# Kernel tuning notes

Hardware: AMD Instinct MI355X
Metric: run time of the kernel (lower is better)

Reference implementation:

```python
import jax, jax.numpy as jnp
import numpy as np

B, S, D = 4, 2048, 1024
H = 4 * D          # expert hidden dim
E_SPEC = 4         # num specific experts
E_SHR = 2          # num shared experts
TOP_K = 2


def setup_inputs() -> dict:
    key = jax.random.key(0)
    ks = jax.random.split(key, 16)
    s = 0.02
    return {
        "x": jax.random.normal(ks[0], (B, S, D), jnp.float32),
        # specific experts (stacked over expert axis)
        "spec_w1": jax.random.normal(ks[1], (E_SPEC, D, H), jnp.float32) * s,
        "spec_b1": jnp.zeros((E_SPEC, H), jnp.float32),
        "spec_w2": jax.random.normal(ks[2], (E_SPEC, H, D), jnp.float32) * s,
        "spec_b2": jnp.zeros((E_SPEC, D), jnp.float32),
        "spec_rw": jax.random.normal(ks[3], (D, E_SPEC), jnp.float32) * s,
        "spec_rb": jnp.zeros((E_SPEC,), jnp.float32),
        # shared experts
        "shr_w1": jax.random.normal(ks[4], (E_SHR, D, H), jnp.float32) * s,
        "shr_b1": jnp.zeros((E_SHR, H), jnp.float32),
        "shr_w2": jax.random.normal(ks[5], (E_SHR, H, D), jnp.float32) * s,
        "shr_b2": jnp.zeros((E_SHR, D), jnp.float32),
        "shr_rw": jax.random.normal(ks[6], (D, E_SHR), jnp.float32) * s,
        "shr_rb": jnp.zeros((E_SHR,), jnp.float32),
    }


def _expert_mlp(xf, w1, b1, w2, b2):
    # xf: [T, D]; w1: [E, D, H]; w2: [E, H, D] -> [E, T, D]
    h = jax.nn.gelu(jnp.einsum("td,edh->eth", xf, w1) + b1[:, None, :],
                    approximate=False)
    return jnp.einsum("eth,ehd->etd", h, w2) + b2[:, None, :]


def reference(x, spec_w1, spec_b1, spec_w2, spec_b2, spec_rw, spec_rb,
              shr_w1, shr_b1, shr_w2, shr_b2, shr_rw, shr_rb):
    b, s, d = x.shape
    xf = x.reshape(-1, d)                      # [T, D]
    T = xf.shape[0]

    # --- specific (top-k) routing ---
    spec_probs = jax.nn.softmax(xf @ spec_rw + spec_rb, axis=-1)   # [T, E]
    topk_probs, topk_idx = jax.lax.top_k(spec_probs, TOP_K)        # [T, K]

    # aux load-balancing loss
    counts = jnp.zeros((E_SPEC,), jnp.float32).at[topk_idx.reshape(-1)].add(1.0)
    fraction = counts / (T * TOP_K)
    aux_loss = E_SPEC * jnp.sum(fraction * spec_probs.mean(axis=0))

    # gate[t, e] = sum_k topk_probs[t,k] * 1[topk_idx[t,k]==e]
    gate = jnp.sum(jax.nn.one_hot(topk_idx, E_SPEC, dtype=xf.dtype)
                   * topk_probs[..., None], axis=1)                # [T, E]

    spec_out_e = _expert_mlp(xf, spec_w1, spec_b1, spec_w2, spec_b2)  # [E, T, D]
    specific_out = jnp.einsum("te,etd->td", gate, spec_out_e)

    # --- shared (dense) experts ---
    shr_probs = jax.nn.softmax(xf @ shr_rw + shr_rb, axis=-1)      # [T, E_shr]
    shr_out_e = _expert_mlp(xf, shr_w1, shr_b1, shr_w2, shr_b2)    # [E_shr, T, D]
    shared_out = jnp.einsum("te,etd->td", shr_probs, shr_out_e)

    final = (specific_out + shared_out).reshape(b, s, d)
    return final, aux_loss
```

## Files before the change

### kernel.cpp

```cpp
#include <hip/hip_runtime.h>
#include <hip/hip_bf16.h>

#define T_TOK 8192
#define DDIM 1024
#define HDIM 4096

typedef __bf16 bf16;
typedef bf16 bf16x8 __attribute__((ext_vector_type(8)));
typedef float f32x4 __attribute__((ext_vector_type(4)));

#define ASM_VMCNT(n) asm volatile("s_waitcnt vmcnt(" #n ")" ::: "memory")
#define MFMA16(a, b, c) __builtin_amdgcn_mfma_f32_16x16x32_bf16((a), (b), (c), 0, 0, 0)

__device__ __forceinline__ void gl_lds16(const void* g, void* l) {
  __builtin_amdgcn_global_load_lds(
      (const __attribute__((address_space(1))) unsigned int*)g,
      (__attribute__((address_space(3))) unsigned int*)l, 16, 0, 0);
}

__device__ __forceinline__ float gelu_f(float v) {
  const float x = v * 0.7071067811865475f;
  const float ax = fabsf(x);
  const float t = 1.0f / fmaf(0.3275911f, ax, 1.0f);
  float p = fmaf(1.061405429f, t, -1.453152027f);
  p = fmaf(p, t, 1.421413741f);
  p = fmaf(p, t, -0.284496736f);
  p = fmaf(p, t, 0.254829592f);
  p = p * t;
  const float e = __expf(-ax * ax);
  const float er = fmaf(-p, e, 1.0f);
  const float erfx = (x >= 0.0f) ? er : -er;
  return 0.5f * v * (1.0f + erfx);
}

__global__ __launch_bounds__(256) void conv_router(
    const float* __restrict__ x, bf16* __restrict__ xb,
    const float* __restrict__ srw, const float* __restrict__ srb,
    const float* __restrict__ hrw, const float* __restrict__ hrb,
    float* __restrict__ gate, float4* __restrict__ probs4,
    int* __restrict__ top2) {
  const int lane = threadIdx.x & 63;
  const int w = threadIdx.x >> 6;
  const int t = blockIdx.x * 4 + w;

  const float* xr = x + (size_t)t * DDIM;
  bf16* xbr = xb + (size_t)t * DDIM;
  float p0 = 0, p1 = 0, p2 = 0, p3 = 0, p4 = 0, p5 = 0;
#pragma unroll
  for (int c = 0; c < 4; ++c) {
    const int d = c * 256 + lane * 4;
    const float4 xv = *(const float4*)(xr + d);
    bf16 ov[4] = {(bf16)xv.x, (bf16)xv.y, (bf16)xv.z, (bf16)xv.w};
    *(float2*)(xbr + d) = *(float2*)ov;
    const float xa[4] = {xv.x, xv.y, xv.z, xv.w};
#pragma unroll
    for (int j = 0; j < 4; ++j) {
      const float xd = xa[j];
      const float4 r4 = *(const float4*)(srw + (size_t)(d + j) * 4);
      p0 += xd * r4.x; p1 += xd * r4.y; p2 += xd * r4.z; p3 += xd * r4.w;
      const float2 r2 = *(const float2*)(hrw + (size_t)(d + j) * 2);
      p4 += xd * r2.x; p5 += xd * r2.y;
    }
  }
#pragma unroll
  for (int off = 32; off >= 1; off >>= 1) {
    p0 += __shfl_xor(p0, off);
    p1 += __shfl_xor(p1, off);
    p2 += __shfl_xor(p2, off);
    p3 += __shfl_xor(p3, off);
    p4 += __shfl_xor(p4, off);
    p5 += __shfl_xor(p5, off);
  }
  if (lane == 0) {
    const float l0 = p0 + srb[0], l1 = p1 + srb[1];
    const float l2 = p2 + srb[2], l3 = p3 + srb[3];
    const float m = fmaxf(fmaxf(l0, l1), fmaxf(l2, l3));
    const float e0 = expf(l0 - m), e1 = expf(l1 - m);
    const float e2 = expf(l2 - m), e3 = expf(l3 - m);
    const float s = e0 + e1 + e2 + e3;
    float pr[4] = {e0 / s, e1 / s, e2 / s, e3 / s};
    int i1 = 0; float v1 = pr[0];
#pragma unroll
    for (int e = 1; e < 4; ++e) if (pr[e] > v1) { v1 = pr[e]; i1 = e; }
    int i2 = -1; float v2 = -1.0f;
#pragma unroll
    for (int e = 0; e < 4; ++e)
      if (e != i1 && pr[e] > v2) { v2 = pr[e]; i2 = e; }
    float g[4] = {0, 0, 0, 0};
    g[i1] = v1; g[i2] = v2;
    float* gr = gate + (size_t)t * 8;
    gr[0] = g[0]; gr[1] = g[1]; gr[2] = g[2]; gr[3] = g[3];
    const float h0 = p4 + hrb[0], h1 = p5 + hrb[1];
    const float mh = fmaxf(h0, h1);
    const float q0 = expf(h0 - mh), q1 = expf(h1 - mh);
    const float qs = q0 + q1;
    gr[4] = q0 / qs; gr[5] = q1 / qs; gr[6] = 0; gr[7] = 0;
    probs4[t] = make_float4(pr[0], pr[1], pr[2], pr[3]);
    top2[t] = i1 | (i2 << 8);
  }
}

__global__ __launch_bounds__(256) void transpose_convert(
    const float* __restrict__ src, bf16* __restrict__ dst, int R, int C) {
  __shared__ float tile[32][33];
  const size_t mat = (size_t)blockIdx.z * R * C;
  const int c0 = blockIdx.x * 32, r0 = blockIdx.y * 32;
  const int tx = threadIdx.x & 31, ty = threadIdx.x >> 5;
#pragma unroll
  for (int i = 0; i < 4; ++i)
    tile[ty + 8 * i][tx] =
        src[mat + (size_t)(r0 + ty + 8 * i) * C + c0 + tx];
  __syncthreads();
#pragma unroll
  for (int i = 0; i < 4; ++i)
    dst[mat + (size_t)(c0 + ty + 8 * i) * R + r0 + tx] =
        (bf16)tile[tx][ty + 8 * i];
}

__global__ __launch_bounds__(1024) void scan_build(
    const int* __restrict__ top2, const float4* __restrict__ probs4,
    int* __restrict__ cnt, int* __restrict__ lists, float* __restrict__ auxg) {
  __shared__ unsigned long long sc[1024];
  __shared__ float4 rp[512];
  const int tid = threadIdx.x;

  int ee[8];
  unsigned long long c = 0;
  float4 ps = make_float4(0.f, 0.f, 0.f, 0.f);
#pragma unroll
  for (int j = 0; j < 8; ++j) {
    const int t = tid * 8 + j;
    const int p = top2[t];
    ee[j] = p;
    const int a = p & 15, b = (p >> 8) & 15;
    c += (1ULL << (16 * a)) + (1ULL << (16 * b));
    const float4 pv = probs4[t];
    ps.x += pv.x; ps.y += pv.y; ps.z += pv.z; ps.w += pv.w;
  }
  sc[tid] = c;
  __syncthreads();
  for (int off = 1; off < 1024; off <<= 1) {
    const unsigned long long mine = sc[tid];
    const unsigned long long prev = (tid >= off) ? sc[tid - off] : 0ULL;
    __syncthreads();
    sc[tid] = mine + prev;
    __syncthreads();
  }
  const unsigned long long incl = sc[tid];
  const unsigned long long tot = sc[1023];
  const unsigned long long excl = incl - c;
  int q0 = (int)(excl & 0xffff), q1 = (int)((excl >> 16) & 0xffff);
  int q2 = (int)((excl >> 32) & 0xffff), q3 = (int)((excl >> 48) & 0xffff);
#pragma unroll
  for (int j = 0; j < 8; ++j) {
    const int t = tid * 8 + j;
    const int a = ee[j] & 15, b = (ee[j] >> 8) & 15;
    const int pa = (a == 0) ? q0 : (a == 1) ? q1 : (a == 2) ? q2 : q3;
    lists[a * 8192 + pa] = t;
    q0 += (a == 0); q1 += (a == 1); q2 += (a == 2); q3 += (a == 3);
    const int pb = (b == 0) ? q0 : (b == 1) ? q1 : (b == 2) ? q2 : q3;
    lists[b * 8192 + pb] = t;
    q0 += (b == 0); q1 += (b == 1); q2 += (b == 2); q3 += (b == 3);
  }
  if (tid == 1023) {
    const int c0 = (int)(tot & 0xffff), c1 = (int)((tot >> 16) & 0xffff);
    const int c2 = (int)((tot >> 32) & 0xffff), c3 = (int)((tot >> 48) & 0xffff);
    cnt[0] = c0; cnt[1] = c1; cnt[2] = c2; cnt[3] = c3;
    auxg[0] = (float)c0; auxg[1] = (float)c1;
    auxg[2] = (float)c2; auxg[3] = (float)c3;
  }
  if (tid >= 512) rp[tid - 512] = ps;
  __syncthreads();
  if (tid < 512) {
    const float4 o = rp[tid];
    ps.x += o.x; ps.y += o.y; ps.z += o.z; ps.w += o.w;
  }
  for (int w = 256; w >= 1; w >>= 1) {
    __syncthreads();
    if (tid >= w && tid < 2 * w) rp[tid - w] = ps;
    __syncthreads();
    if (tid < w) {
      const float4 o = rp[tid];
      ps.x += o.x; ps.y += o.y; ps.z += o.z; ps.w += o.w;
    }
  }
  if (tid == 0) {
    auxg[4] = ps.x; auxg[5] = ps.y; auxg[6] = ps.z; auxg[7] = ps.w;
  }
}

__global__ void aux_finalize(const float* __restrict__ auxg,
                             float* __restrict__ outp) {
  float a = 0.0f;
#pragma unroll
  for (int e = 0; e < 4; ++e)
    a += (auxg[e] / (float)(T_TOK * 2)) * (auxg[4 + e] / (float)T_TOK);
  outp[0] = 4.0f * a;
}

template <int MODE>
__global__ __launch_bounds__(256, 2) void gemmw(
    const bf16* __restrict__ A, const bf16* __restrict__ B, int N, int K,
    const float* __restrict__ bias, bf16* __restrict__ Hout, int NBn,
    int CH_M, int CH_N, const int* __restrict__ cnt,
    const int* __restrict__ lists, int eid) {
  __shared__ __align__(1024) bf16 As[3 * 256 * 32];
  __shared__ __align__(1024) bf16 Bs[3 * 128 * 32];

  const int tid = threadIdx.x;
  const int lane = tid & 63, wid = tid >> 6;
  const int wm = wid >> 1, wn = wid & 1;
  const int lr = lane & 15, lg = lane >> 4;

  int bm, bn;
  if constexpr (MODE == 4) {
    const int nbm = ((cnt[eid] + 255) & ~255) >> 8;
    const int CHm = (nbm + 3) >> 2;
    const int need = 8 * CHm * CH_N;
    if (blockIdx.x >= need) return;
    const int xc = blockIdx.x & 7;
    const int idx = blockIdx.x >> 3;
    bm = (xc >> 1) * CHm + idx / CH_N;
    bn = (xc & 1) * CH_N + idx % CH_N;
    if (bm >= nbm) return;
  } else {
    const int xcd = blockIdx.x & 7;
    const int idx = blockIdx.x >> 3;
    const int ncn = NBn / CH_N;
    bm = (xcd / ncn) * CH_M + idx / CH_N;
    bn = (xcd % ncn) * CH_N + idx % CH_N;
  }

  const int rl = tid >> 2;
  const int c = ((tid & 3) * 16) ^ (((rl >> 1) & 3) << 4);
  int ar0 = bm * 256 + rl, ar1 = ar0 + 64, ar2 = ar0 + 128, ar3 = ar0 + 192;
  if constexpr (MODE == 4) {
    const int* lp = lists + eid * 8192;
    int t;
    t = lp[ar0]; ar0 = t < 0 ? 0 : t;
    t = lp[ar1]; ar1 = t < 0 ? 0 : t;
    t = lp[ar2]; ar2 = t < 0 ? 0 : t;
    t = lp[ar3]; ar3 = t < 0 ? 0 : t;
  }
  const bf16* sA0 = A + (size_t)ar0 * K + (c >> 1);
  const bf16* sA1 = A + (size_t)ar1 * K + (c >> 1);
  const bf16* sA2 = A + (size_t)ar2 * K + (c >> 1);
  const bf16* sA3 = A + (size_t)ar3 * K + (c >> 1);
  const bf16* sB0 = B + (size_t)(bn * 128 + rl) * K + (c >> 1);
  const bf16* sB1 = B + (size_t)(bn * 128 + 64 + rl) * K + (c >> 1);

  char* const dA = (char*)As + wid * 1024;
  char* const dB = (char*)Bs + wid * 1024;

  const int rkey = ((lr >> 1) & 3) << 4;
  const char* Ard = (const char*)As + (wm * 128 + lr) * 64 + ((lg * 16) ^ rkey);
  const char* Brd = (const char*)Bs + (wn * 64 + lr) * 64 + ((lg * 16) ^ rkey);

  f32x4 acc[8][4] = {};
  const int NT = K >> 5;

#define GW_STAGE(KO, SLOT)                         \
  gl_lds16(sA0 + (KO), dA + (SLOT)*16384);         \
  gl_lds16(sA1 + (KO), dA + (SLOT)*16384 + 4096);  \
  gl_lds16(sA2 + (KO), dA + (SLOT)*16384 + 8192);  \
  gl_lds16(sA3 + (KO), dA + (SLOT)*16384 + 12288); \
  gl_lds16(sB0 + (KO), dB + (SLOT)*8192);          \
  gl_lds16(sB1 + (KO), dB + (SLOT)*8192 + 4096);
  GW_STAGE(0, 0)
  GW_STAGE(32, 1)
  GW_STAGE(64, 2)
  ASM_VMCNT(12);
  __builtin_amdgcn_s_barrier();

#define GW_ITER(KT, SLOT)                                                  \
  {                                                                        \
    bf16x8 af[8], bfr[4];                                                  \
    _Pragma("unroll") for (int mf = 0; mf < 8; ++mf)                       \
        af[mf] = *(const bf16x8*)(Ard + (SLOT)*16384 + mf * 1024);         \
    _Pragma("unroll") for (int nf = 0; nf < 4; ++nf)                       \
        bfr[nf] = *(const bf16x8*)(Brd + (SLOT)*8192 + nf * 1024);         \
    asm volatile("s_waitcnt lgkmcnt(0)" ::: "memory");                     \
    __builtin_amdgcn_s_setprio(1);                                         \
    _Pragma("unroll") for (int mf = 0; mf < 8; ++mf)                       \
        _Pragma("unroll") for (int nf = 0; nf < 4; ++nf)                   \
            acc[mf][nf] = MFMA16(af[mf], bfr[nf], acc[mf][nf]);            \
    __builtin_amdgcn_s_setprio(0);                                         \
    __builtin_amdgcn_s_barrier();                                          \
    if ((KT) + 3 < NT) {                                                   \
      const int ko_ = ((KT) + 3) << 5;                                     \
      GW_STAGE(ko_, SLOT)                                                  \
      ASM_VMCNT(12);                                                       \
    } else if ((KT) + 2 < NT) {                                            \
      ASM_VMCNT(6);                                                        \
    } else if ((KT) + 1 < NT) {                                            \
      ASM_VMCNT(0);                                                        \
    }                                                                      \
    __builtin_amdgcn_s_barrier();                                          \
  }

  for (int kt0 = 0; kt0 < NT; kt0 += 3) {
    GW_ITER(kt0, 0)
    if (kt0 + 1 < NT) GW_ITER(kt0 + 1, 1)
    if (kt0 + 2 < NT) GW_ITER(kt0 + 2, 2)
  }

  const int colb = bn * 128 + wn * 64;
  const int rowb = bm * 256 + wm * 128 + lg * 4;
  float bv[4];
#pragma unroll
  for (int nf = 0; nf < 4; ++nf) bv[nf] = bias[colb + nf * 16 + lr];
#pragma unroll
  for (int mf = 0; mf < 8; ++mf)
#pragma unroll
    for (int nf = 0; nf < 4; ++nf) {
      const int col = colb + nf * 16 + lr;
#pragma unroll
      for (int r = 0; r < 4; ++r) {
        const int row = rowb + mf * 16 + r;
        Hout[(size_t)row * N + col] = (bf16)gelu_f(acc[mf][nf][r] + bv[nf]);
      }
    }
}

template <int BN_, int MODE>
__global__ __launch_bounds__(512, 2) void gemm4p(
    const bf16* __restrict__ A, const bf16* __restrict__ B, int M, int N,
    int K, const float* __restrict__ bias, bf16* __restrict__ Hout,
    float* __restrict__ Fout, const float* __restrict__ gate, int gidx,
    int NBn, int CH_M, int CH_N, const int* __restrict__ cnt,
    const int* __restrict__ lists, int eid) {
  constexpr int NREP = BN_ / 64;
  constexpr int NHF = NREP / 2;
  constexpr int WNT = BN_ / 4;
  constexpr int ABYTES = 256 * 64 * 2;
  constexpr int BBYTES = BN_ * 64 * 2;
  constexpr bool DYN = (MODE == 3);

  __shared__ __align__(1024) bf16 Alds[2 * 256 * 64];
  __shared__ __align__(1024) bf16 Blds[2 * BN_ * 64];

  const int tid = threadIdx.x;
  const int lane = tid & 63, wid = tid >> 6;
  const int wm = wid >> 2, wn = wid & 3;
  const int lr = lane & 15, lg = lane >> 4;

  int bm, bn;
  if constexpr (DYN) {
    const int nbm = ((cnt[eid] + 255) & ~255) >> 8;
    const int CHm = (nbm + 3) >> 2;
    constexpr int CHn = (BN_ == 256) ? 8 : 4;
    const int need = 8 * CHm * CHn;
    if (blockIdx.x >= need) return;
    const int xc = blockIdx.x & 7;
    const int idx = blockIdx.x >> 3;
    bm = (xc >> 1) * CHm + idx / CHn;
    bn = (xc & 1) * CHn + idx % CHn;
    if (bm >= nbm) return;
  } else {
    const int xcd = blockIdx.x & 7;
    const int idx = blockIdx.x >> 3;
    const int ncn = NBn / CH_N;
    bm = (xcd / ncn) * CH_M + idx / CH_N;
    bn = (xcd % ncn) * CH_N + idx % CH_N;
  }

  const int NT = K >> 6;

  const int L = tid * 16;
  const int rl = L >> 7;
  const int colb = (L & 127) ^ ((rl & 7) << 4);

  const int ar0 = bm * 256 + rl;
  const bf16* sAc0 = A + (size_t)ar0 * K + (colb >> 1);
  const bf16* sAc1 = A + (size_t)(ar0 + 64) * K + (colb >> 1);
  const bf16* sAc2 = A + (size_t)(ar0 + 128) * K + (colb >> 1);
  const bf16* sAc3 = A + (size_t)(ar0 + 192) * K + (colb >> 1);
  const bf16* sB = B + (size_t)(bn * BN_ + rl) * K + (colb >> 1);

  char* const ldsA = (char*)Alds;
  char* const ldsB = (char*)Blds;
  const int wb = wid * 1024;
  char* const stA[2] = {ldsA + wb, ldsA + ABYTES + wb};
  char* const stB[2] = {ldsB + wb, ldsB + BBYTES + wb};

  const int ax0 = (lg * 16) ^ ((lr & 7) << 4);
  const int ax1 = ax0 ^ 64;
  const int aro = (wm * 128 + lr) * 128;
  const int bro = (wn * WNT + lr) * 128;
  const char* const Ak0[2] = {ldsA + aro + ax0, ldsA + ABYTES + aro + ax0};
  const char* const Ak1[2] = {ldsA + aro + ax1, ldsA + ABYTES + aro + ax1};
  const char* const Bk0[2] = {ldsB + bro + ax0, ldsB + BBYTES + bro + ax0};
  const char* const Bk1[2] = {ldsB + bro + ax1, ldsB + BBYTES + bro + ax1};

  f32x4 acc[8][NREP] = {};

  gl_lds16(sAc0, stA[0]);
  gl_lds16(sAc1, stA[0] + 8192);
  gl_lds16(sAc2, stA[0] + 16384);
  gl_lds16(sAc3, stA[0] + 24576);
  gl_lds16(sB, stB[0]);
  gl_lds16(sB + (size_t)64 * K, stB[0] + 8192);
  if constexpr (BN_ == 256) {
    gl_lds16(sB + (size_t)128 * K, stB[0] + 16384);
    gl_lds16(sB + (size_t)192 * K, stB[0] + 24576);
  }
  gl_lds16(sB + 64, stB[1]);
  gl_lds16(sB + (size_t)64 * K + 64, stB[1] + 8192);
  if constexpr (BN_ == 256) {
    gl_lds16(sB + (size_t)128 * K + 64, stB[1] + 16384);
    gl_lds16(sB + (size_t)192 * K + 64, stB[1] + 24576);
  }
  gl_lds16(sAc0 + 64, stA[1]);
  gl_lds16(sAc1 + 64, stA[1] + 8192);
  if constexpr (BN_ == 256) ASM_VMCNT(6); else ASM_VMCNT(4);
  __builtin_amdgcn_s_barrier();

  for (int kt0 = 0; kt0 < NT; kt0 += 2) {
#pragma unroll
    for (int par = 0; par < 2; ++par) {
      const int kt = kt0 + par;
      const int cur = par, oth = par ^ 1;
      const bool st1 = (kt + 1) < NT, st2 = (kt + 2) < NT;
      const size_t ko1 = (size_t)(kt + 1) << 6, ko2 = (size_t)(kt + 2) << 6;
      const char* Ac0 = Ak0[cur]; const char* Ac1 = Ak1[cur];
      const char* Bc0 = Bk0[cur]; const char* Bc1 = Bk1[cur];

      bf16x8 af[4][2], bfr[NREP][2];

#pragma unroll
      for (int mf = 0; mf < 4; ++mf) {
        af[mf][0] = *(const bf16x8*)(Ac0 + mf * 2048);
        af[mf][1] = *(const bf16x8*)(Ac1 + mf * 2048);
      }
#pragma unroll
      for (int nf = 0; nf < NHF; ++nf) {
        bfr[nf][0] = *(const bf16x8*)(Bc0 + nf * 2048);
        bfr[nf][1] = *(const bf16x8*)(Bc1 + nf * 2048);
      }
      if (st1) {
        gl_lds16(sAc2 + ko1, stA[oth] + 16384);
        gl_lds16(sAc3 + ko1, stA[oth] + 24576);
      }
      __builtin_amdgcn_s_barrier();
      asm volatile("s_waitcnt lgkmcnt(0)" ::: "memory");
      __builtin_amdgcn_sched_barrier(0);
      __builtin_amdgcn_s_setprio(1);
#pragma unroll
      for (int mf = 0; mf < 4; ++mf)
#pragma unroll
        for (int nf = 0; nf < NHF; ++nf) {
          acc[mf][nf] = MFMA16(af[mf][0], bfr[nf][0], acc[mf][nf]);
          acc[mf][nf] = MFMA16(af[mf][1], bfr[nf][1], acc[mf][nf]);
        }
      __builtin_amdgcn_s_setprio(0);
      __builtin_amdgcn_s_barrier();

#pragma unroll
      for (int nf = NHF; nf < NREP; ++nf) {
        bfr[nf][0] = *(const bf16x8*)(Bc0 + nf * 2048);
        bfr[nf][1] = *(const bf16x8*)(Bc1 + nf * 2048);
      }
      __builtin_amdgcn_s_barrier();
      asm volatile("s_waitcnt lgkmcnt(0)" ::: "memory");
      __builtin_amdgcn_sched_barrier(0);
      __builtin_amdgcn_s_setprio(1);
#pragma unroll
      for (int mf = 0; mf < 4; ++mf)
#pragma unroll
        for (int nf = NHF; nf < NREP; ++nf) {
          acc[mf][nf] = MFMA16(af[mf][0], bfr[nf][0], acc[mf][nf]);
          acc[mf][nf] = MFMA16(af[mf][1], bfr[nf][1], acc[mf][nf]);
        }
      __builtin_amdgcn_s_setprio(0);
      __builtin_amdgcn_s_barrier();

#pragma unroll
      for (int mf = 0; mf < 4; ++mf) {
        af[mf][0] = *(const bf16x8*)(Ac0 + 8192 + mf * 2048);
        af[mf][1] = *(const bf16x8*)(Ac1 + 8192 + mf * 2048);
      }
      if (st2) {
        gl_lds16(sB + ko2, stB[cur]);
        gl_lds16(sB + (size_t)64 * K + ko2, stB[cur] + 8192);
      }
      __builtin_amdgcn_s_barrier();
      asm volatile("s_waitcnt lgkmcnt(0)" ::: "memory");
      __builtin_amdgcn_sched_barrier(0);
      __builtin_amdgcn_s_setprio(1);
#pragma unroll
      for (int mf = 0; mf < 4; ++mf)
#pragma unroll
        for (int nf = 0; nf < NHF; ++nf) {
          acc[4 + mf][nf] = MFMA16(af[mf][0], bfr[nf][0], acc[4 + mf][nf]);
          acc[4 + mf][nf] = MFMA16(af[mf][1], bfr[nf][1], acc[4 + mf][nf]);
        }
      __builtin_amdgcn_s_setprio(0);
      __builtin_amdgcn_s_barrier();

      if (st2) {
        if constexpr (BN_ == 256) {
          gl_lds16(sB + (size_t)128 * K + ko2, stB[cur] + 16384);
          gl_lds16(sB + (size_t)192 * K + ko2, stB[cur] + 24576);
        }
        gl_lds16(sAc0 + ko2, stA[cur]);
        gl_lds16(sAc1 + ko2, stA[cur] + 8192);
      }
      __builtin_amdgcn_s_setprio(1);
#pragma unroll
      for (int mf = 0; mf < 4; ++mf)
#pragma unroll
        for (int nf = NHF; nf < NREP; ++nf) {
          acc[4 + mf][nf] = MFMA16(af[mf][0], bfr[nf][0], acc[4 + mf][nf]);
          acc[4 + mf][nf] = MFMA16(af[mf][1], bfr[nf][1], acc[4 + mf][nf]);
        }
      __builtin_amdgcn_s_setprio(0);
      if (st2) {
        if constexpr (BN_ == 256) ASM_VMCNT(6); else ASM_VMCNT(4);
        __builtin_amdgcn_s_barrier();
      } else if (st1) {
        ASM_VMCNT(0);
        __builtin_amdgcn_s_barrier();
      }
    }
  }

  const int colb2 = bn * BN_ + wn * WNT;
  const int rowb = bm * 256 + wm * 128 + lg * 4;
  float bv[NREP];
#pragma unroll
  for (int nf = 0; nf < NREP; ++nf) bv[nf] = bias[colb2 + nf * 16 + lr];
#pragma unroll
  for (int mf = 0; mf < 8; ++mf) {
    if constexpr (MODE == 1 || MODE == 2) {
      float gv[4];
#pragma unroll
      for (int r = 0; r < 4; ++r)
        gv[r] = gate[(size_t)(rowb + mf * 16 + r) * 8 + gidx];
#pragma unroll
      for (int nf = 0; nf < NREP; ++nf) {
        const int col = colb2 + nf * 16 + lr;
#pragma unroll
        for (int r = 0; r < 4; ++r) {
          const float v = acc[mf][nf][r] + bv[nf];
          const size_t oi = (size_t)(rowb + mf * 16 + r) * N + col;
          if constexpr (MODE == 1)
            Fout[oi] += gv[r] * v;
          else
            Fout[oi] = gv[r] * v;
        }
      }
    } else {
      const int* lp = lists + eid * 8192;
      int tok[4]; float gv[4];
#pragma unroll
      for (int r = 0; r < 4; ++r) {
        tok[r] = lp[rowb + mf * 16 + r];
        gv[r] = tok[r] >= 0 ? gate[(size_t)tok[r] * 8 + gidx] : 0.0f;
      }
#pragma unroll
      for (int nf = 0; nf < NREP; ++nf) {
        const int col = colb2 + nf * 16 + lr;
#pragma unroll
        for (int r = 0; r < 4; ++r) {
          if (tok[r] >= 0) {
            const float v = acc[mf][nf][r] + bv[nf];
            Fout[(size_t)tok[r] * N + col] += gv[r] * v;
          }
        }
      }
    }
  }
}

extern "C" void kernel_launch(void* const* d_in, const int* in_sizes, int n_in,
                              void* d_out, int out_size, void* d_ws,
                              size_t ws_size, hipStream_t stream) {
  const float* x = (const float*)d_in[0];
  const float* spec_w1 = (const float*)d_in[1];
  const float* spec_b1 = (const float*)d_in[2];
  const float* spec_w2 = (const float*)d_in[3];
  const float* spec_b2 = (const float*)d_in[4];
  const float* spec_rw = (const float*)d_in[5];
  const float* spec_rb = (const float*)d_in[6];
  const float* shr_w1 = (const float*)d_in[7];
  const float* shr_b1 = (const float*)d_in[8];
  const float* shr_w2 = (const float*)d_in[9];
  const float* shr_b2 = (const float*)d_in[10];
  const float* shr_rw = (const float*)d_in[11];
  const float* shr_rb = (const float*)d_in[12];
  float* out = (float*)d_out;

  char* ws = (char*)d_ws;
  const size_t OFF_W1 = 16777216;
  const size_t OFF_W2 = OFF_W1 + 50331648;
  const size_t OFF_H = OFF_W2 + 50331648;
  const size_t OFF_GATE = OFF_H + 67108864;
  const size_t OFF_AUX = OFF_GATE + 262144;
  const size_t OFF_CNT = OFF_AUX + 64;
  const size_t OFF_LIST = OFF_CNT + 64;
  const size_t OFF_T2 = OFF_LIST + 131072;
  const size_t OFF_P4 = OFF_T2 + 32768;
  bf16* xb = (bf16*)ws;
  bf16* w1t = (bf16*)(ws + OFF_W1);
  bf16* w2t = (bf16*)(ws + OFF_W2);
  bf16* hbuf = (bf16*)(ws + OFF_H);
  float* gate = (float*)(ws + OFF_GATE);
  float* auxg = (float*)(ws + OFF_AUX);
  int* cnt = (int*)(ws + OFF_CNT);
  int* lists = (int*)(ws + OFF_LIST);
  int* top2 = (int*)(ws + OFF_T2);
  float4* probs4 = (float4*)(ws + OFF_P4);

  hipMemsetAsync(lists, 0xFF, 4 * 8192 * 4, stream);

  conv_router<<<T_TOK / 4, 256, 0, stream>>>(x, xb, spec_rw, spec_rb, shr_rw,
                                             shr_rb, gate, probs4, top2);
  scan_build<<<1, 1024, 0, stream>>>(top2, probs4, cnt, lists, auxg);

  transpose_convert<<<dim3(HDIM / 32, DDIM / 32, 4), 256, 0, stream>>>(
      spec_w1, w1t, DDIM, HDIM);
  transpose_convert<<<dim3(HDIM / 32, DDIM / 32, 2), 256, 0, stream>>>(
      shr_w1, w1t + (size_t)4 * DDIM * HDIM, DDIM, HDIM);
  transpose_convert<<<dim3(DDIM / 32, HDIM / 32, 4), 256, 0, stream>>>(
      spec_w2, w2t, HDIM, DDIM);
  transpose_convert<<<dim3(DDIM / 32, HDIM / 32, 2), 256, 0, stream>>>(
      shr_w2, w2t + (size_t)4 * DDIM * HDIM, HDIM, DDIM);

  for (int es = 0; es < 2; ++es) {
    const bf16* w1e = w1t + (size_t)(4 + es) * DDIM * HDIM;
    const bf16* w2e = w2t + (size_t)(4 + es) * DDIM * HDIM;
    const float* b1e = shr_b1 + (size_t)es * HDIM;
    const float* b2e = shr_b2 + (size_t)es * DDIM;
    gemmw<0><<<1024, 256, 0, stream>>>(xb, w1e, HDIM, DDIM, b1e, hbuf,
                                       32, 8, 16, nullptr, nullptr, 0);
    if (es == 0)
      gemm4p<128, 2><<<256, 512, 0, stream>>>(
          hbuf, w2e, T_TOK, DDIM, HDIM, b2e, nullptr, out, gate, 4,
          8, 8, 4, nullptr, nullptr, 0);
    else
      gemm4p<128, 1><<<256, 512, 0, stream>>>(
          hbuf, w2e, T_TOK, DDIM, HDIM, b2e, nullptr, out, gate, 5,
          8, 8, 4, nullptr, nullptr, 0);
  }

  for (int e = 0; e < 4; ++e) {
    const bf16* w1e = w1t + (size_t)e * DDIM * HDIM;
    const bf16* w2e = w2t + (size_t)e * DDIM * HDIM;
    const float* b1e = spec_b1 + (size_t)e * HDIM;
    const float* b2e = spec_b2 + (size_t)e * DDIM;
    gemmw<4><<<1024, 256, 0, stream>>>(xb, w1e, HDIM, DDIM, b1e, hbuf,
                                       32, 0, 16, cnt, lists, e);
    gemm4p<128, 3><<<256, 512, 0, stream>>>(
        hbuf, w2e, T_TOK, DDIM, HDIM, b2e, nullptr, out, gate, e,
        8, 0, 0, cnt, lists, e);
  }
  aux_finalize<<<1, 1, 0, stream>>>(auxg, out + (size_t)T_TOK * DDIM);
}
```

Measured before the change: 1.054 ms.

## Batch all six expert GEMMs into two grouped launches with atomic accumulation

Replaces the twelve per-expert GEMM launches with one grouped first-layer GEMM and one grouped second-layer GEMM. A metadata table built in the scan kernel maps each block to its expert and to a packed hidden-buffer offset. Outputs are accumulated with atomicAdd into a zero-initialised output, and the weight transposes are merged into two launches. The aim is to remove launch gaps and partial-wave tails between experts. In exchange it needs a much larger hidden buffer and adds float atomic traffic and nondeterministic summation order; when the workspace is too small it falls back to per-expert launches.

```diff
diff --git a/kernel.cpp b/kernel.cpp
--- a/kernel.cpp
+++ b/kernel.cpp
@@ -100,26 +100,29 @@
   }
 }
 
-__global__ __launch_bounds__(256) void transpose_convert(
-    const float* __restrict__ src, bf16* __restrict__ dst, int R, int C) {
+__global__ __launch_bounds__(256) void transpose_convert6(
+    const float* __restrict__ spec_w, const float* __restrict__ shr_w,
+    bf16* __restrict__ dst, int R, int C) {
   __shared__ float tile[32][33];
-  const size_t mat = (size_t)blockIdx.z * R * C;
+  const int z = blockIdx.z;
+  const float* src = (z < 4) ? spec_w + (size_t)z * R * C
+                             : shr_w + (size_t)(z - 4) * R * C;
+  bf16* d = dst + (size_t)z * R * C;
   const int c0 = blockIdx.x * 32, r0 = blockIdx.y * 32;
   const int tx = threadIdx.x & 31, ty = threadIdx.x >> 5;
 #pragma unroll
   for (int i = 0; i < 4; ++i)
-    tile[ty + 8 * i][tx] =
-        src[mat + (size_t)(r0 + ty + 8 * i) * C + c0 + tx];
+    tile[ty + 8 * i][tx] = src[(size_t)(r0 + ty + 8 * i) * C + c0 + tx];
   __syncthreads();
 #pragma unroll
   for (int i = 0; i < 4; ++i)
-    dst[mat + (size_t)(c0 + ty + 8 * i) * R + r0 + tx] =
-        (bf16)tile[tx][ty + 8 * i];
+    d[(size_t)(c0 + ty + 8 * i) * R + r0 + tx] = (bf16)tile[tx][ty + 8 * i];
 }
 
 __global__ __launch_bounds__(1024) void scan_build(
     const int* __restrict__ top2, const float4* __restrict__ probs4,
-    int* __restrict__ cnt, int* __restrict__ lists, float* __restrict__ auxg) {
+    int* __restrict__ meta, int* __restrict__ lists,
+    float* __restrict__ auxg) {
   __shared__ unsigned long long sc[1024];
   __shared__ float4 rp[512];
   const int tid = threadIdx.x;
@@ -165,9 +168,27 @@
   if (tid == 1023) {
     const int c0 = (int)(tot & 0xffff), c1 = (int)((tot >> 16) & 0xffff);
     const int c2 = (int)((tot >> 32) & 0xffff), c3 = (int)((tot >> 48) & 0xffff);
-    cnt[0] = c0; cnt[1] = c1; cnt[2] = c2; cnt[3] = c3;
+    meta[24] = c0; meta[25] = c1; meta[26] = c2; meta[27] = c3;
     auxg[0] = (float)c0; auxg[1] = (float)c1;
     auxg[2] = (float)c2; auxg[3] = (float)c3;
+    const int nb0 = (c0 + 255) >> 8, nb1 = (c1 + 255) >> 8;
+    const int nb2 = (c2 + 255) >> 8, nb3 = (c3 + 255) >> 8;
+    const int ch0 = (nb0 + 3) >> 2, ch1 = (nb1 + 3) >> 2;
+    const int ch2 = (nb2 + 3) >> 2, ch3 = (nb3 + 3) >> 2;
+    meta[0] = 0; meta[1] = 1024; meta[2] = 2048;
+    meta[3] = 2048 + 128 * ch0;
+    meta[4] = meta[3] + 128 * ch1;
+    meta[5] = meta[4] + 128 * ch2;
+    meta[6] = meta[5] + 128 * ch3;
+    meta[8] = 0; meta[9] = 256; meta[10] = 512;
+    meta[11] = 512 + 32 * ch0;
+    meta[12] = meta[11] + 32 * ch1;
+    meta[13] = meta[12] + 32 * ch2;
+    meta[14] = meta[13] + 32 * ch3;
+    meta[16] = 0; meta[17] = 8192; meta[18] = 16384;
+    meta[19] = 16384 + nb0 * 256;
+    meta[20] = meta[19] + nb1 * 256;
+    meta[21] = meta[20] + nb2 * 256;
   }
   if (tid >= 512) rp[tid - 512] = ps;
   __syncthreads();
@@ -198,12 +219,11 @@
   outp[0] = 4.0f * a;
 }
 
-template <int MODE>
-__global__ __launch_bounds__(256, 2) void gemmw(
-    const bf16* __restrict__ A, const bf16* __restrict__ B, int N, int K,
-    const float* __restrict__ bias, bf16* __restrict__ Hout, int NBn,
-    int CH_M, int CH_N, const int* __restrict__ cnt,
-    const int* __restrict__ lists, int eid) {
+__global__ __launch_bounds__(256, 2) void g1_batched(
+    const bf16* __restrict__ A, const bf16* __restrict__ w1t,
+    const float* __restrict__ spec_b1, const float* __restrict__ shr_b1,
+    bf16* __restrict__ h_all, const int* __restrict__ meta,
+    const int* __restrict__ lists, int s_only, int packed) {
   __shared__ __align__(1024) bf16 As[3 * 256 * 32];
   __shared__ __align__(1024) bf16 Bs[3 * 128 * 32];
 
@@ -212,30 +232,44 @@
   const int wm = wid >> 1, wn = wid & 1;
   const int lr = lane & 15, lg = lane >> 4;
 
-  int bm, bn;
-  if constexpr (MODE == 4) {
-    const int nbm = ((cnt[eid] + 255) & ~255) >> 8;
+  int s, local;
+  if (s_only >= 0) {
+    s = s_only; local = blockIdx.x;
+  } else {
+    const int b = blockIdx.x;
+    if (b >= meta[6]) return;
+    s = 0;
+#pragma unroll
+    for (int i = 1; i < 6; ++i) s += (b >= meta[i]);
+    local = b - meta[s];
+  }
+
+  int bm, bn, nbm = 32;
+  if (s < 2) {
+    if (local >= 1024) return;
+    const int xcd = local & 7, idx = local >> 3;
+    bm = (xcd >> 1) * 8 + idx / 16;
+    bn = (xcd & 1) * 16 + idx % 16;
+  } else {
+    nbm = (meta[24 + s - 2] + 255) >> 8;
     const int CHm = (nbm + 3) >> 2;
-    const int need = 8 * CHm * CH_N;
-    if (blockIdx.x >= need) return;
-    const int xc = blockIdx.x & 7;
-    const int idx = blockIdx.x >> 3;
-    bm = (xc >> 1) * CHm + idx / CH_N;
-    bn = (xc & 1) * CH_N + idx % CH_N;
+    if (local >= 8 * CHm * 16) return;
+    const int xc = local & 7, idx = local >> 3;
+    bm = (xc >> 1) * CHm + idx / 16;
+    bn = (xc & 1) * 16 + idx % 16;
     if (bm >= nbm) return;
-  } else {
-    const int xcd = blockIdx.x & 7;
-    const int idx = blockIdx.x >> 3;
-    const int ncn = NBn / CH_N;
-    bm = (xcd / ncn) * CH_M + idx / CH_N;
-    bn = (xcd % ncn) * CH_N + idx % CH_N;
-  }
+  }
+  const int hb = packed ? meta[16 + s] : 0;
+  const bf16* B = w1t + (size_t)(s < 2 ? 4 + s : s - 2) * DDIM * HDIM;
+  const float* bias = (s < 2) ? shr_b1 + (size_t)s * HDIM
+                              : spec_b1 + (size_t)(s - 2) * HDIM;
+  const int K = DDIM, N = HDIM;
 
   const int rl = tid >> 2;
   const int c = ((tid & 3) * 16) ^ (((rl >> 1) & 3) << 4);
   int ar0 = bm * 256 + rl, ar1 = ar0 + 64, ar2 = ar0 + 128, ar3 = ar0 + 192;
-  if constexpr (MODE == 4) {
-    const int* lp = lists + eid * 8192;
+  if (s >= 2) {
+    const int* lp = lists + (s - 2) * 8192;
     int t;
     t = lp[ar0]; ar0 = t < 0 ? 0 : t;
     t = lp[ar1]; ar1 = t < 0 ? 0 : t;
@@ -305,7 +339,7 @@
   }
 
   const int colb = bn * 128 + wn * 64;
-  const int rowb = bm * 256 + wm * 128 + lg * 4;
+  const int rowb = hb + bm * 256 + wm * 128 + lg * 4;
   float bv[4];
 #pragma unroll
   for (int nf = 0; nf < 4; ++nf) bv[nf] = bias[colb + nf * 16 + lr];
@@ -317,82 +351,87 @@
 #pragma unroll
       for (int r = 0; r < 4; ++r) {
         const int row = rowb + mf * 16 + r;
-        Hout[(size_t)row * N + col] = (bf16)gelu_f(acc[mf][nf][r] + bv[nf]);
+        h_all[(size_t)row * N + col] = (bf16)gelu_f(acc[mf][nf][r] + bv[nf]);
       }
     }
 }
 
-template <int BN_, int MODE>
-__global__ __launch_bounds__(512, 2) void gemm4p(
-    const bf16* __restrict__ A, const bf16* __restrict__ B, int M, int N,
-    int K, const float* __restrict__ bias, bf16* __restrict__ Hout,
-    float* __restrict__ Fout, const float* __restrict__ gate, int gidx,
-    int NBn, int CH_M, int CH_N, const int* __restrict__ cnt,
-    const int* __restrict__ lists, int eid) {
-  constexpr int NREP = BN_ / 64;
-  constexpr int NHF = NREP / 2;
-  constexpr int WNT = BN_ / 4;
-  constexpr int ABYTES = 256 * 64 * 2;
-  constexpr int BBYTES = BN_ * 64 * 2;
-  constexpr bool DYN = (MODE == 3);
-
+__global__ __launch_bounds__(512, 2) void g2_batched(
+    const bf16* __restrict__ h_all, const bf16* __restrict__ w2t,
+    const float* __restrict__ spec_b2, const float* __restrict__ shr_b2,
+    float* __restrict__ out, const float* __restrict__ gate,
+    const int* __restrict__ meta, const int* __restrict__ lists,
+    int s_only, int packed) {
   __shared__ __align__(1024) bf16 Alds[2 * 256 * 64];
-  __shared__ __align__(1024) bf16 Blds[2 * BN_ * 64];
+  __shared__ __align__(1024) bf16 Blds[2 * 128 * 64];
 
   const int tid = threadIdx.x;
   const int lane = tid & 63, wid = tid >> 6;
   const int wm = wid >> 2, wn = wid & 3;
   const int lr = lane & 15, lg = lane >> 4;
 
-  int bm, bn;
-  if constexpr (DYN) {
-    const int nbm = ((cnt[eid] + 255) & ~255) >> 8;
+  int s, local;
+  if (s_only >= 0) {
+    s = s_only; local = blockIdx.x;
+  } else {
+    const int b = blockIdx.x;
+    if (b >= meta[14]) return;
+    s = 0;
+#pragma unroll
+    for (int i = 9; i < 14; ++i) s += (b >= meta[i]);
+    local = b - meta[8 + s];
+  }
+
+  int bm, bn, nbm = 32;
+  if (s < 2) {
+    if (local >= 256) return;
+    const int xcd = local & 7, idx = local >> 3;
+    bm = (xcd >> 1) * 8 + idx / 4;
+    bn = (xcd & 1) * 4 + idx % 4;
+  } else {
+    nbm = (meta[24 + s - 2] + 255) >> 8;
     const int CHm = (nbm + 3) >> 2;
-    constexpr int CHn = (BN_ == 256) ? 8 : 4;
-    const int need = 8 * CHm * CHn;
-    if (blockIdx.x >= need) return;
-    const int xc = blockIdx.x & 7;
-    const int idx = blockIdx.x >> 3;
-    bm = (xc >> 1) * CHm + idx / CHn;
-    bn = (xc & 1) * CHn + idx % CHn;
+    if (local >= 8 * CHm * 4) return;
+    const int xc = local & 7, idx = local >> 3;
+    bm = (xc >> 1) * CHm + idx / 4;
+    bn = (xc & 1) * 4 + idx % 4;
     if (bm >= nbm) return;
-  } else {
-    const int xcd = blockIdx.x & 7;
-    const int idx = blockIdx.x >> 3;
-    const int ncn = NBn / CH_N;
-    bm = (xcd / ncn) * CH_M + idx / CH_N;
-    bn = (xcd % ncn) * CH_N + idx % CH_N;
-  }
-
+  }
+  const int hb = packed ? meta[16 + s] : 0;
+  const bf16* B = w2t + (size_t)(s < 2 ? 4 + s : s - 2) * DDIM * HDIM;
+  const float* bias = (s < 2) ? shr_b2 + (size_t)s * DDIM
+                              : spec_b2 + (size_t)(s - 2) * DDIM;
+  const int gidx = (s < 2) ? 4 + s : s - 2;
+  const int K = HDIM, N = DDIM;
   const int NT = K >> 6;
 
   const int L = tid * 16;
   const int rl = L >> 7;
   const int colb = (L & 127) ^ ((rl & 7) << 4);
 
-  const int ar0 = bm * 256 + rl;
-  const bf16* sAc0 = A + (size_t)ar0 * K + (colb >> 1);
-  const bf16* sAc1 = A + (size_t)(ar0 + 64) * K + (colb >> 1);
-  const bf16* sAc2 = A + (size_t)(ar0 + 128) * K + (colb >> 1);
-  const bf16* sAc3 = A + (size_t)(ar0 + 192) * K + (colb >> 1);
-  const bf16* sB = B + (size_t)(bn * BN_ + rl) * K + (colb >> 1);
+  const int ar0 = hb + bm * 256 + rl;
+  const bf16* sAc0 = h_all + (size_t)ar0 * K + (colb >> 1);
+  const bf16* sAc1 = h_all + (size_t)(ar0 + 64) * K + (colb >> 1);
+  const bf16* sAc2 = h_all + (size_t)(ar0 + 128) * K + (colb >> 1);
+  const bf16* sAc3 = h_all + (size_t)(ar0 + 192) * K + (colb >> 1);
+  const bf16* sB = B + (size_t)(bn * 128 + rl) * K + (colb >> 1);
 
   char* const ldsA = (char*)Alds;
   char* const ldsB = (char*)Blds;
   const int wb = wid * 1024;
-  char* const stA[2] = {ldsA + wb, ldsA + ABYTES + wb};
-  char* const stB[2] = {ldsB + wb, ldsB + BBYTES + wb};
+  char* const stA[2] = {ldsA + wb, ldsA + 32768 + wb};
+  char* const stB[2] = {ldsB + wb, ldsB + 16384 + wb};
 
   const int ax0 = (lg * 16) ^ ((lr & 7) << 4);
   const int ax1 = ax0 ^ 64;
   const int aro = (wm * 128 + lr) * 128;
-  const int bro = (wn * WNT + lr) * 128;
-  const char* const Ak0[2] = {ldsA + aro + ax0, ldsA + ABYTES + aro + ax0};
-  const char* const Ak1[2] = {ldsA + aro + ax1, ldsA + ABYTES + aro + ax1};
-  const char* const Bk0[2] = {ldsB + bro + ax0, ldsB + BBYTES + bro + ax0};
-  const char* const Bk1[2] = {ldsB + bro + ax1, ldsB + BBYTES + bro + ax1};
-
-  f32x4 acc[8][NREP] = {};
+  const int bro = (wn * 32 + lr) * 128;
+  const char* const Ak0[2] = {ldsA + aro + ax0, ldsA + 32768 + aro + ax0};
+  const char* const Ak1[2] = {ldsA + aro + ax1, ldsA + 32768 + aro + ax1};
+  const char* const Bk0[2] = {ldsB + bro + ax0, ldsB + 16384 + bro + ax0};
+  const char* const Bk1[2] = {ldsB + bro + ax1, ldsB + 16384 + bro + ax1};
+
+  f32x4 acc[8][2] = {};
 
   gl_lds16(sAc0, stA[0]);
   gl_lds16(sAc1, stA[0] + 8192);
@@ -400,19 +439,11 @@
   gl_lds16(sAc3, stA[0] + 24576);
   gl_lds16(sB, stB[0]);
   gl_lds16(sB + (size_t)64 * K, stB[0] + 8192);
-  if constexpr (BN_ == 256) {
-    gl_lds16(sB + (size_t)128 * K, stB[0] + 16384);
-    gl_lds16(sB + (size_t)192 * K, stB[0] + 24576);
-  }
   gl_lds16(sB + 64, stB[1]);
   gl_lds16(sB + (size_t)64 * K + 64, stB[1] + 8192);
-  if constexpr (BN_ == 256) {
-    gl_lds16(sB + (size_t)128 * K + 64, stB[1] + 16384);
-    gl_lds16(sB + (size_t)192 * K + 64, stB[1] + 24576);
-  }
   gl_lds16(sAc0 + 64, stA[1]);
   gl_lds16(sAc1 + 64, stA[1] + 8192);
-  if constexpr (BN_ == 256) ASM_VMCNT(6); else ASM_VMCNT(4);
+  ASM_VMCNT(4);
   __builtin_amdgcn_s_barrier();
 
   for (int kt0 = 0; kt0 < NT; kt0 += 2) {
@@ -425,18 +456,15 @@
       const char* Ac0 = Ak0[cur]; const char* Ac1 = Ak1[cur];
       const char* Bc0 = Bk0[cur]; const char* Bc1 = Bk1[cur];
 
-      bf16x8 af[4][2], bfr[NREP][2];
+      bf16x8 af[4][2], bfr[2][2];
 
 #pragma unroll
       for (int mf = 0; mf < 4; ++mf) {
         af[mf][0] = *(const bf16x8*)(Ac0 + mf * 2048);
         af[mf][1] = *(const bf16x8*)(Ac1 + mf * 2048);
       }
-#pragma unroll
-      for (int nf = 0; nf < NHF; ++nf) {
-        bfr[nf][0] = *(const bf16x8*)(Bc0 + nf * 2048);
-        bfr[nf][1] = *(const bf16x8*)(Bc1 + nf * 2048);
-      }
+      bfr[0][0] = *(const bf16x8*)(Bc0);
+      bfr[0][1] = *(const bf16x8*)(Bc1);
       if (st1) {
         gl_lds16(sAc2 + ko1, stA[oth] + 16384);
         gl_lds16(sAc3 + ko1, stA[oth] + 24576);
@@ -446,31 +474,24 @@
       __builtin_amdgcn_sched_barrier(0);
       __builtin_amdgcn_s_setprio(1);
 #pragma unroll
-      for (int mf = 0; mf < 4; ++mf)
-#pragma unroll
-        for (int nf = 0; nf < NHF; ++nf) {
-          acc[mf][nf] = MFMA16(af[mf][0], bfr[nf][0], acc[mf][nf]);
-          acc[mf][nf] = MFMA16(af[mf][1], bfr[nf][1], acc[mf][nf]);
-        }
+      for (int mf = 0; mf < 4; ++mf) {
+        acc[mf][0] = MFMA16(af[mf][0], bfr[0][0], acc[mf][0]);
+        acc[mf][0] = MFMA16(af[mf][1], bfr[0][1], acc[mf][0]);
+      }
       __builtin_amdgcn_s_setprio(0);
       __builtin_amdgcn_s_barrier();
 
-#pragma unroll
-      for (int nf = NHF; nf < NREP; ++nf) {
-        bfr[nf][0] = *(const bf16x8*)(Bc0 + nf * 2048);
-        bfr[nf][1] = *(const bf16x8*)(Bc1 + nf * 2048);
-      }
+      bfr[1][0] = *(const bf16x8*)(Bc0 + 2048);
+      bfr[1][1] = *(const bf16x8*)(Bc1 + 2048);
       __builtin_amdgcn_s_barrier();
       asm volatile("s_waitcnt lgkmcnt(0)" ::: "memory");
       __builtin_amdgcn_sched_barrier(0);
       __builtin_amdgcn_s_setprio(1);
 #pragma unroll
-      for (int mf = 0; mf < 4; ++mf)
-#pragma unroll
-        for (int nf = NHF; nf < NREP; ++nf) {
-          acc[mf][nf] = MFMA16(af[mf][0], bfr[nf][0], acc[mf][nf]);
-          acc[mf][nf] = MFMA16(af[mf][1], bfr[nf][1], acc[mf][nf]);
-        }
+      for (int mf = 0; mf < 4; ++mf) {
+        acc[mf][1] = MFMA16(af[mf][0], bfr[1][0], acc[mf][1]);
+        acc[mf][1] = MFMA16(af[mf][1], bfr[1][1], acc[mf][1]);
+      }
       __builtin_amdgcn_s_setprio(0);
       __builtin_amdgcn_s_barrier();
 
@@ -488,34 +509,26 @@
       __builtin_amdgcn_sched_barrier(0);
       __builtin_amdgcn_s_setprio(1);
 #pragma unroll
-      for (int mf = 0; mf < 4; ++mf)
-#pragma unroll
-        for (int nf = 0; nf < NHF; ++nf) {
-          acc[4 + mf][nf] = MFMA16(af[mf][0], bfr[nf][0], acc[4 + mf][nf]);
-          acc[4 + mf][nf] = MFMA16(af[mf][1], bfr[nf][1], acc[4 + mf][nf]);
-        }
+      for (int mf = 0; mf < 4; ++mf) {
+        acc[4 + mf][0] = MFMA16(af[mf][0], bfr[0][0], acc[4 + mf][0]);
+        acc[4 + mf][0] = MFMA16(af[mf][1], bfr[0][1], acc[4 + mf][0]);
+      }
       __builtin_amdgcn_s_setprio(0);
       __builtin_amdgcn_s_barrier();
 
       if (st2) {
-        if constexpr (BN_ == 256) {
-          gl_lds16(sB + (size_t)128 * K + ko2, stB[cur] + 16384);
-          gl_lds16(sB + (size_t)192 * K + ko2, stB[cur] + 24576);
-        }
         gl_lds16(sAc0 + ko2, stA[cur]);
         gl_lds16(sAc1 + ko2, stA[cur] + 8192);
       }
       __builtin_amdgcn_s_setprio(1);
 #pragma unroll
-      for (int mf = 0; mf < 4; ++mf)
-#pragma unroll
-        for (int nf = NHF; nf < NREP; ++nf) {
-          acc[4 + mf][nf] = MFMA16(af[mf][0], bfr[nf][0], acc[4 + mf][nf]);
-          acc[4 + mf][nf] = MFMA16(af[mf][1], bfr[nf][1], acc[4 + mf][nf]);
-        }
+      for (int mf = 0; mf < 4; ++mf) {
+        acc[4 + mf][1] = MFMA16(af[mf][0], bfr[1][0], acc[4 + mf][1]);
+        acc[4 + mf][1] = MFMA16(af[mf][1], bfr[1][1], acc[4 + mf][1]);
+      }
       __builtin_amdgcn_s_setprio(0);
       if (st2) {
-        if constexpr (BN_ == 256) ASM_VMCNT(6); else ASM_VMCNT(4);
+        ASM_VMCNT(4);
         __builtin_amdgcn_s_barrier();
       } else if (st1) {
         ASM_VMCNT(0);
@@ -524,48 +537,28 @@
     }
   }
 
-  const int colb2 = bn * BN_ + wn * WNT;
+  const int colb2 = bn * 128 + wn * 32;
   const int rowb = bm * 256 + wm * 128 + lg * 4;
-  float bv[NREP];
-#pragma unroll
-  for (int nf = 0; nf < NREP; ++nf) bv[nf] = bias[colb2 + nf * 16 + lr];
+  float bv[2];
+#pragma unroll
+  for (int nf = 0; nf < 2; ++nf) bv[nf] = bias[colb2 + nf * 16 + lr];
 #pragma unroll
   for (int mf = 0; mf < 8; ++mf) {
-    if constexpr (MODE == 1 || MODE == 2) {
-      float gv[4];
-#pragma unroll
-      for (int r = 0; r < 4; ++r)
-        gv[r] = gate[(size_t)(rowb + mf * 16 + r) * 8 + gidx];
-#pragma unroll
-      for (int nf = 0; nf < NREP; ++nf) {
-        const int col = colb2 + nf * 16 + lr;
-#pragma unroll
-        for (int r = 0; r < 4; ++r) {
+    int tok[4]; float gv[4];
+#pragma unroll
+    for (int r = 0; r < 4; ++r) {
+      const int lrow = rowb + mf * 16 + r;
+      tok[r] = (s < 2) ? lrow : lists[(s - 2) * 8192 + lrow];
+      gv[r] = tok[r] >= 0 ? gate[(size_t)tok[r] * 8 + gidx] : 0.0f;
+    }
+#pragma unroll
+    for (int nf = 0; nf < 2; ++nf) {
+      const int col = colb2 + nf * 16 + lr;
+#pragma unroll
+      for (int r = 0; r < 4; ++r) {
+        if (tok[r] >= 0) {
           const float v = acc[mf][nf][r] + bv[nf];
-          const size_t oi = (size_t)(rowb + mf * 16 + r) * N + col;
-          if constexpr (MODE == 1)
-            Fout[oi] += gv[r] * v;
-          else
-            Fout[oi] = gv[r] * v;
-        }
-      }
-    } else {
-      const int* lp = lists + eid * 8192;
-      int tok[4]; float gv[4];
-#pragma unroll
-      for (int r = 0; r < 4; ++r) {
-        tok[r] = lp[rowb + mf * 16 + r];
-        gv[r] = tok[r] >= 0 ? gate[(size_t)tok[r] * 8 + gidx] : 0.0f;
-      }
-#pragma unroll
-      for (int nf = 0; nf < NREP; ++nf) {
-        const int col = colb2 + nf * 16 + lr;
-#pragma unroll
-        for (int r = 0; r < 4; ++r) {
-          if (tok[r] >= 0) {
-            const float v = acc[mf][nf][r] + bv[nf];
-            Fout[(size_t)tok[r] * N + col] += gv[r] * v;
-          }
+          atomicAdd(&out[(size_t)tok[r] * N + col], gv[r] * v);
         }
       }
     }
@@ -593,66 +586,51 @@
   char* ws = (char*)d_ws;
   const size_t OFF_W1 = 16777216;
   const size_t OFF_W2 = OFF_W1 + 50331648;
-  const size_t OFF_H = OFF_W2 + 50331648;
-  const size_t OFF_GATE = OFF_H + 67108864;
+  const size_t OFF_GATE = OFF_W2 + 50331648;
   const size_t OFF_AUX = OFF_GATE + 262144;
-  const size_t OFF_CNT = OFF_AUX + 64;
-  const size_t OFF_LIST = OFF_CNT + 64;
+  const size_t OFF_META = OFF_AUX + 256;
+  const size_t OFF_LIST = OFF_META + 256;
   const size_t OFF_T2 = OFF_LIST + 131072;
   const size_t OFF_P4 = OFF_T2 + 32768;
+  const size_t OFF_H = OFF_P4 + 131072 + 1024;
   bf16* xb = (bf16*)ws;
   bf16* w1t = (bf16*)(ws + OFF_W1);
   bf16* w2t = (bf16*)(ws + OFF_W2);
-  bf16* hbuf = (bf16*)(ws + OFF_H);
   float* gate = (float*)(ws + OFF_GATE);
   float* auxg = (float*)(ws + OFF_AUX);
-  int* cnt = (int*)(ws + OFF_CNT);
+  int* meta = (int*)(ws + OFF_META);
   int* lists = (int*)(ws + OFF_LIST);
   int* top2 = (int*)(ws + OFF_T2);
   float4* probs4 = (float4*)(ws + OFF_P4);
-
+  bf16* h_all = (bf16*)(ws + OFF_H);
+
+  const size_t H_GRAND = (size_t)34048 * HDIM * 2;
+  const bool grand = ws_size >= OFF_H + H_GRAND;
+
+  hipMemsetAsync(out, 0, (size_t)T_TOK * DDIM * 4, stream);
   hipMemsetAsync(lists, 0xFF, 4 * 8192 * 4, stream);
 
   conv_router<<<T_TOK / 4, 256, 0, stream>>>(x, xb, spec_rw, spec_rb, shr_rw,
                                              shr_rb, gate, probs4, top2);
-  scan_build<<<1, 1024, 0, stream>>>(top2, probs4, cnt, lists, auxg);
-
-  transpose_convert<<<dim3(HDIM / 32, DDIM / 32, 4), 256, 0, stream>>>(
-      spec_w1, w1t, DDIM, HDIM);
-  transpose_convert<<<dim3(HDIM / 32, DDIM / 32, 2), 256, 0, stream>>>(
-      shr_w1, w1t + (size_t)4 * DDIM * HDIM, DDIM, HDIM);
-  transpose_convert<<<dim3(DDIM / 32, HDIM / 32, 4), 256, 0, stream>>>(
-      spec_w2, w2t, HDIM, DDIM);
-  transpose_convert<<<dim3(DDIM / 32, HDIM / 32, 2), 256, 0, stream>>>(
-      shr_w2, w2t + (size_t)4 * DDIM * HDIM, HDIM, DDIM);
-
-  for (int es = 0; es < 2; ++es) {
-    const bf16* w1e = w1t + (size_t)(4 + es) * DDIM * HDIM;
-    const bf16* w2e = w2t + (size_t)(4 + es) * DDIM * HDIM;
-    const float* b1e = shr_b1 + (size_t)es * HDIM;
-    const float* b2e = shr_b2 + (size_t)es * DDIM;
-    gemmw<0><<<1024, 256, 0, stream>>>(xb, w1e, HDIM, DDIM, b1e, hbuf,
-                                       32, 8, 16, nullptr, nullptr, 0);
-    if (es == 0)
-      gemm4p<128, 2><<<256, 512, 0, stream>>>(
-          hbuf, w2e, T_TOK, DDIM, HDIM, b2e, nullptr, out, gate, 4,
-          8, 8, 4, nullptr, nullptr, 0);
-    else
-      gemm4p<128, 1><<<256, 512, 0, stream>>>(
-          hbuf, w2e, T_TOK, DDIM, HDIM, b2e, nullptr, out, gate, 5,
-          8, 8, 4, nullptr, nullptr, 0);
-  }
-
-  for (int e = 0; e < 4; ++e) {
-    const bf16* w1e = w1t + (size_t)e * DDIM * HDIM;
-    const bf16* w2e = w2t + (size_t)e * DDIM * HDIM;
-    const float* b1e = spec_b1 + (size_t)e * HDIM;
-    const float* b2e = spec_b2 + (size_t)e * DDIM;
-    gemmw<4><<<1024, 256, 0, stream>>>(xb, w1e, HDIM, DDIM, b1e, hbuf,
-                                       32, 0, 16, cnt, lists, e);
-    gemm4p<128, 3><<<256, 512, 0, stream>>>(
-        hbuf, w2e, T_TOK, DDIM, HDIM, b2e, nullptr, out, gate, e,
-        8, 0, 0, cnt, lists, e);
+  scan_build<<<1, 1024, 0, stream>>>(top2, probs4, meta, lists, auxg);
+
+  transpose_convert6<<<dim3(HDIM / 32, DDIM / 32, 6), 256, 0, stream>>>(
+      spec_w1, shr_w1, w1t, DDIM, HDIM);
+  transpose_convert6<<<dim3(DDIM / 32, HDIM / 32, 6), 256, 0, stream>>>(
+      spec_w2, shr_w2, w2t, HDIM, DDIM);
+
+  if (grand) {
+    g1_batched<<<5120, 256, 0, stream>>>(xb, w1t, spec_b1, shr_b1, h_all,
+                                         meta, lists, -1, 1);
+    g2_batched<<<1280, 512, 0, stream>>>(h_all, w2t, spec_b2, shr_b2, out,
+                                         gate, meta, lists, -1, 1);
+  } else {
+    for (int s = 0; s < 6; ++s) {
+      g1_batched<<<1024, 256, 0, stream>>>(xb, w1t, spec_b1, shr_b1, h_all,
+                                           meta, lists, s, 0);
+      g2_batched<<<256, 512, 0, stream>>>(h_all, w2t, spec_b2, shr_b2, out,
+                                          gate, meta, lists, s, 0);
+    }
   }
   aux_finalize<<<1, 1, 0, stream>>>(auxg, out + (size_t)T_TOK * DDIM);
 }
```

Result: slower. 1.105 ms (+4.8%).
